# Performance work log

Hardware: AMD Instinct MI355X
Metric: run time of the kernel (lower is better)

## Reference

```python
import jax, jax.numpy as jnp
import numpy as np

B, T, DIM, H = 4, 2048, 1024, 16
HD = DIM // H  # 64
ROPE_BASE = 10000.0


def _rope_cos_sin(seq_len, head_dim, dtype):
    # lucidrains rotary-embedding-torch convention: interleaved pairs.
    inv_freq = 1.0 / (ROPE_BASE ** (jnp.arange(0, head_dim, 2, dtype=jnp.float32) / head_dim))
    freqs = jnp.arange(seq_len, dtype=jnp.float32)[:, None] * inv_freq[None, :]  # [T, hd/2]
    freqs = jnp.repeat(freqs, 2, axis=-1)  # [T, hd], each freq duplicated for the pair
    return jnp.cos(freqs).astype(dtype), jnp.sin(freqs).astype(dtype)


def _rotate_half(x):
    # interleaved pairs: (x1, x2) -> (-x2, x1)
    x = x.reshape(*x.shape[:-1], -1, 2)
    x1, x2 = x[..., 0], x[..., 1]
    return jnp.stack([-x2, x1], axis=-1).reshape(*x.shape[:-2], -1)


def _apply_rope(x, cos, sin):
    # x: [B, H, T, hd]; cos/sin: [T, hd]
    return x * cos[None, None, :, :] + _rotate_half(x) * sin[None, None, :, :]


def setup_inputs() -> dict:
    key = jax.random.key(0)
    kx, kqkv, kw, kb = jax.random.split(key, 4)
    s_qkv = 1.0 / np.sqrt(DIM)
    return {
        "x": jax.random.normal(kx, (B, T, DIM), dtype=jnp.float32),
        "w_qkv": jax.random.normal(kqkv, (3 * DIM, DIM), dtype=jnp.float32) * s_qkv,
        "w_proj": jax.random.normal(kw, (DIM, DIM), dtype=jnp.float32) * s_qkv,
        "b_proj": jax.random.normal(kb, (DIM,), dtype=jnp.float32) * 0.01,
    }


def reference(x, w_qkv, w_proj, b_proj):
    b, t, c = x.shape
    qkv = jnp.einsum('btc,dc->btd', x, w_qkv)  # [B, T, 3*C]
    qkv = qkv.reshape(b, t, 3, H, HD).transpose(2, 0, 3, 1, 4)  # [3, B, H, T, hd]
    q, k, v = qkv[0], qkv[1], qkv[2]

    cos, sin = _rope_cos_sin(t, HD, x.dtype)
    q = _apply_rope(q, cos, sin)
    k = _apply_rope(k, cos, sin)

    scale = 1.0 / np.sqrt(HD)
    scores = jnp.einsum('bhqd,bhkd->bhqk', q, k) * scale  # [B, H, T, T]
    attn = jax.nn.softmax(scores, axis=-1)
    out = jnp.einsum('bhqk,bhkd->bhqd', attn, v)  # [B, H, T, hd]

    out = out.transpose(0, 2, 1, 3).reshape(b, t, c)  # [B, T, C]
    return jnp.einsum('btc,dc->btd', out, w_proj) + b_proj
```

## Files before the change

kernel.cpp:

```cpp
#include <hip/hip_runtime.h>
#include <hip/hip_bf16.h>
#include <math.h>

#define Bz   4
#define Tz   2048
#define DIMz 1024
#define Hz   16
#define HDz  64
#define BHz  (Bz*Hz)
#define Mz   (Bz*Tz)
#define LOG2E 1.44269504088896340736f
#define QSCALE (0.125f * LOG2E)

typedef __attribute__((ext_vector_type(8)))  __bf16 bf16x8;
typedef __attribute__((ext_vector_type(4)))  __bf16 bf16x4;
typedef __attribute__((ext_vector_type(2)))  __bf16 bf16x2;
typedef __attribute__((ext_vector_type(4)))  float  f32x4;
typedef __attribute__((ext_vector_type(16))) float  f32x16;

__device__ __forceinline__ f32x4 mfma_16x16x32(bf16x8 a, bf16x8 b, f32x4 c) {
  return __builtin_amdgcn_mfma_f32_16x16x32_bf16(a, b, c, 0, 0, 0);
}
__device__ __forceinline__ f32x16 mfma_32x32x16(bf16x8 a, bf16x8 b, f32x16 c) {
  return __builtin_amdgcn_mfma_f32_32x32x16_bf16(a, b, c, 0, 0, 0);
}

__device__ __forceinline__ ushort f2bf(float f) {
  unsigned u = __float_as_uint(f);
  u += 0x7fffu + ((u >> 16) & 1u);
  return (ushort)(u >> 16);
}

__device__ __forceinline__ void gl_lds16(const ushort* g, ushort* l) {
  __builtin_amdgcn_global_load_lds(
      (const __attribute__((address_space(1))) unsigned int*)g,
      (__attribute__((address_space(3))) unsigned int*)l, 16, 0, 0);
}

#define N4_X   (Mz * DIMz / 4)
#define N4_WQ  (3 * DIMz * DIMz / 4)
#define N4_WP  (DIMz * DIMz / 4)
__global__ void k_cvt3(const float4* __restrict__ x,  ushort4* __restrict__ ox,
                       const float4* __restrict__ wq, ushort4* __restrict__ owq,
                       const float4* __restrict__ wp, ushort4* __restrict__ owp) {
  int i = blockIdx.x * blockDim.x + threadIdx.x;
  const float4* in; ushort4* out;
  if (i < N4_X)                { in = x + i;                 out = ox + i; }
  else if (i < N4_X + N4_WQ)   { in = wq + (i - N4_X);       out = owq + (i - N4_X); }
  else if (i < N4_X + N4_WQ + N4_WP) { in = wp + (i - N4_X - N4_WQ); out = owp + (i - N4_X - N4_WQ); }
  else return;
  float4 v = *in;
  ushort4 o;
  o.x = f2bf(v.x); o.y = f2bf(v.y); o.z = f2bf(v.z); o.w = f2bf(v.w);
  *out = o;
}

__global__ void k_rope_tab(float* __restrict__ tab) {
  int idx = blockIdx.x * blockDim.x + threadIdx.x;
  if (idx >= Tz * 32) return;
  int t = idx >> 5, i = idx & 31;
  double ang = (double)t * exp(((double)(-2 * i) / (double)HDz) * log(10000.0));
  tab[2 * idx]     = (float)cos(ang);
  tab[2 * idx + 1] = (float)sin(ang);
}


__global__ __launch_bounds__(256) void k_gemm_qkv(const ushort* __restrict__ A,
                                                  const ushort* __restrict__ Bw,
                                                  const float* __restrict__ tab,
                                                  ushort* __restrict__ qb,
                                                  ushort* __restrict__ kb,
                                                  ushort* __restrict__ vbt) {
  __shared__ ushort As[128 * 64];
  __shared__ ushort Bs[128 * 64];
  const int tid = threadIdx.x;
  const int bm = (blockIdx.x & 63) << 7;
  const int bn = (blockIdx.x >> 6) << 7;
  const int wid = tid >> 6, lane = tid & 63;
  const int wr = (wid & 1) << 6, wc = (wid >> 1) << 6;
  const int lr = lane & 15, lg = lane >> 4;

  const int r8 = lane >> 3;
  const int cswz = (((lane & 7) ^ r8) << 3);
  const ushort* pA = A  + (size_t)(bm + wid * 8 + r8) * 1024 + cswz;
  const ushort* pB = Bw + (size_t)(bn + wid * 8 + r8) * 1024 + cswz;
  ushort* lA = &As[wid * 512];
  ushort* lB = &Bs[wid * 512];

  const int cs0 = ((lg ^ (lr & 7)) << 3);
  const int cs1 = cs0 ^ 32;

  const f32x4 fz = {0.f, 0.f, 0.f, 0.f};
  f32x4 acc[4][4];
  #pragma unroll
  for (int i = 0; i < 4; i++)
    #pragma unroll
    for (int j = 0; j < 4; j++) acc[i][j] = fz;

  for (int k0 = 0; k0 < 1024; k0 += 64) {
    __syncthreads();
    #pragma unroll
    for (int rep = 0; rep < 4; rep++) {
      gl_lds16(pA + (size_t)rep * 32768 + k0, lA + rep * 2048);
      gl_lds16(pB + (size_t)rep * 32768 + k0, lB + rep * 2048);
    }
    __syncthreads();
    #pragma unroll
    for (int kc = 0; kc < 2; kc++) {
      const int cs = kc ? cs1 : cs0;
      bf16x8 af[4], bfr[4];
      #pragma unroll
      for (int i = 0; i < 4; i++)
        af[i] = *reinterpret_cast<const bf16x8*>(&As[(wr + i * 16 + lr) * 64 + cs]);
      #pragma unroll
      for (int j = 0; j < 4; j++)
        bfr[j] = *reinterpret_cast<const bf16x8*>(&Bs[(wc + j * 16 + lr) * 64 + cs]);
      #pragma unroll
      for (int i = 0; i < 4; i++)
        #pragma unroll
        for (int j = 0; j < 4; j++)
          acc[i][j] = mfma_16x16x32(af[i], bfr[j], acc[i][j]);
    }
  }

  #pragma unroll
  for (int j = 0; j < 4; j++) {
    int col = bn + wc + j * 16 + lr;
    int which = col >> 10;
    int r = col & 1023;
    int h = r >> 6, hd = r & 63;
    #pragma unroll
    for (int i = 0; i < 4; i++) {
      int row0 = bm + wr + i * 16 + lg * 4;
      int b = row0 >> 11, t0 = row0 & 2047;
      if (which == 2) {
        int t0p = (t0 & ~12) | ((t0 & 4) << 1) | ((t0 & 8) >> 1);
        uint lo = (uint)f2bf(acc[i][j][0]) | ((uint)f2bf(acc[i][j][1]) << 16);
        uint hi = (uint)f2bf(acc[i][j][2]) | ((uint)f2bf(acc[i][j][3]) << 16);
        *reinterpret_cast<uint2*>(&vbt[((size_t)(b * Hz + h) * HDz + hd) * Tz + t0p]) =
            make_uint2(lo, hi);
      } else {
        ushort* dst = (which == 0) ? qb : kb;
        const float sc = (which == 0) ? QSCALE : 1.0f;
        const float sgn = (hd & 1) ? 1.0f : -1.0f;
        const float* tb = &tab[((size_t)t0 * 32 + (hd >> 1)) * 2];
        #pragma unroll
        for (int q = 0; q < 4; q++) {
          float own = acc[i][j][q];
          float other = __shfl_xor(own, 1);
          float c = tb[q * 64], s = tb[q * 64 + 1];
          dst[(((size_t)(b * Hz + h) * Tz + t0 + q) << 6) + hd] =
              f2bf((own * c + sgn * other * s) * sc);
        }
      }
    }
  }
}

__global__ __launch_bounds__(256, 4) void k_attn(const ushort* __restrict__ qb,
                                                 const ushort* __restrict__ kbp,
                                                 const ushort* __restrict__ vbt,
                                                 ushort* __restrict__ ao) {
  __shared__ ushort Ks0[64 * 64], Ks1[64 * 64], Ks2[64 * 64];
  __shared__ ushort Vs0[64 * 64], Vs1[64 * 64];

  const int bid = ((blockIdx.x & 7) << 7) + (blockIdx.x >> 3);
  const int qt = bid & 15;
  const int bh = bid >> 4;
  const int tid = threadIdx.x, wid = tid >> 6, lane = tid & 63;
  const int l31 = lane & 31, hi = lane >> 5;

  const ushort* Kg = kbp + (size_t)bh * Tz * HDz;
  const ushort* Vg = vbt + (size_t)bh * HDz * Tz;

  const ushort* Qrow = qb + ((size_t)bh * Tz + qt * 128 + wid * 32 + l31) * HDz + hi * 8;
  bf16x8 qf[4];
  #pragma unroll
  for (int m = 0; m < 4; m++)
    qf[m] = *reinterpret_cast<const bf16x8*>(Qrow + m * 16);

  bf16x8 onev;
  #pragma unroll
  for (int j = 0; j < 8; j++) onev[j] = (__bf16)1.0f;

  const int r8 = lane >> 3;
  const int c0 = (((lane & 7) ^ r8 ^ ((2 * wid) & 3)) << 3);
  const int c1 = (((lane & 7) ^ r8 ^ ((2 * wid + 1) & 3)) << 3);
  const ushort* kp0 = Kg + (size_t)(wid * 16 + r8) * 64 + c0;
  const ushort* kp1 = Kg + (size_t)(wid * 16 + 8 + r8) * 64 + c1;
  const ushort* vp0 = Vg + (size_t)(wid * 16 + r8) * Tz + c0;
  const ushort* vp1 = Vg + (size_t)(wid * 16 + 8 + r8) * Tz + c1;

  f32x16 oacc0, oacc1, lacc;
  #pragma unroll
  for (int i = 0; i < 16; i++) { oacc0[i] = 0.f; oacc1[i] = 0.f; lacc[i] = 0.f; }

  const int swr = (lane & 7) ^ ((lane >> 3) & 3);
  int csk[4];
  #pragma unroll
  for (int m = 0; m < 4; m++) csk[m] = ((2 * m + hi) ^ swr) << 3;

  union FP { uint u[4]; bf16x8 v; };

  ushort *kb_cur = Ks0, *kb_nxt = Ks1, *kb_pre = Ks2;
  ushort *vb_cur = Vs0, *vb_nxt = Vs1;

  gl_lds16(kp0, kb_cur + wid * 1024); gl_lds16(kp1, kb_cur + wid * 1024 + 512);
  gl_lds16(kp0 + 4096, kb_nxt + wid * 1024); gl_lds16(kp1 + 4096, kb_nxt + wid * 1024 + 512);
  gl_lds16(vp0, vb_cur + wid * 1024); gl_lds16(vp1, vb_cur + wid * 1024 + 512);
  asm volatile("s_waitcnt vmcnt(4)" ::: "memory");
  __builtin_amdgcn_s_barrier();

  const int NT = Tz / 64;
  for (int kt = 0; kt < NT; kt++) {
    if (kt + 2 < NT) {
      gl_lds16(kp0 + (size_t)(kt + 2) * 4096, kb_pre + wid * 1024);
      gl_lds16(kp1 + (size_t)(kt + 2) * 4096, kb_pre + wid * 1024 + 512);
    }

    f32x16 sA, sB;
    #pragma unroll
    for (int i = 0; i < 16; i++) { sA[i] = 0.f; sB[i] = 0.f; }
    __builtin_amdgcn_s_setprio(1);
    #pragma unroll
    for (int m = 0; m < 4; m++) {
      bf16x8 kfA = *reinterpret_cast<const bf16x8*>(&kb_cur[l31 * 64 + csk[m]]);
      bf16x8 kfB = *reinterpret_cast<const bf16x8*>(&kb_cur[(32 + l31) * 64 + csk[m]]);
      sA = mfma_32x32x16(kfA, qf[m], sA);
      sB = mfma_32x32x16(kfB, qf[m], sB);
    }
    __builtin_amdgcn_s_setprio(0);

    FP fA0, fA1, fB0, fB1;
    #pragma unroll
    for (int i = 0; i < 4; i++) {
      bf16x2 a0, a1, b0, b1;
      a0[0] = (__bf16)__builtin_exp2f(sA[2 * i]);
      a0[1] = (__bf16)__builtin_exp2f(sA[2 * i + 1]);
      a1[0] = (__bf16)__builtin_exp2f(sA[8 + 2 * i]);
      a1[1] = (__bf16)__builtin_exp2f(sA[9 + 2 * i]);
      b0[0] = (__bf16)__builtin_exp2f(sB[2 * i]);
      b0[1] = (__bf16)__builtin_exp2f(sB[2 * i + 1]);
      b1[0] = (__bf16)__builtin_exp2f(sB[8 + 2 * i]);
      b1[1] = (__bf16)__builtin_exp2f(sB[9 + 2 * i]);
      fA0.u[i] = *reinterpret_cast<uint*>(&a0);
      fA1.u[i] = *reinterpret_cast<uint*>(&a1);
      fB0.u[i] = *reinterpret_cast<uint*>(&b0);
      fB1.u[i] = *reinterpret_cast<uint*>(&b1);
    }

    asm volatile("s_waitcnt vmcnt(2)" ::: "memory");
    __builtin_amdgcn_s_barrier();

    if (kt + 1 < NT) {
      gl_lds16(vp0 + (kt + 1) * 64, vb_nxt + wid * 1024);
      gl_lds16(vp1 + (kt + 1) * 64, vb_nxt + wid * 1024 + 512);
    }

    __builtin_amdgcn_s_setprio(1);
    lacc = mfma_32x32x16(fA0.v, onev, lacc);
    lacc = mfma_32x32x16(fA1.v, onev, lacc);
    lacc = mfma_32x32x16(fB0.v, onev, lacc);
    lacc = mfma_32x32x16(fB1.v, onev, lacc);
    #pragma unroll
    for (int blk = 0; blk < 2; blk++) {
      const ushort* vrow = &vb_cur[(blk * 32 + l31) * 64];
      bf16x8 vf0 = *reinterpret_cast<const bf16x8*>(vrow + csk[0]);
      bf16x8 vf1 = *reinterpret_cast<const bf16x8*>(vrow + csk[1]);
      bf16x8 vf2 = *reinterpret_cast<const bf16x8*>(vrow + csk[2]);
      bf16x8 vf3 = *reinterpret_cast<const bf16x8*>(vrow + csk[3]);
      f32x16 o = blk ? oacc1 : oacc0;
      o = mfma_32x32x16(fA0.v, vf0, o);
      o = mfma_32x32x16(fA1.v, vf1, o);
      o = mfma_32x32x16(fB0.v, vf2, o);
      o = mfma_32x32x16(fB1.v, vf3, o);
      if (blk) oacc1 = o; else oacc0 = o;
    }
    __builtin_amdgcn_s_setprio(0);

    ushort* t0 = kb_cur; kb_cur = kb_nxt; kb_nxt = kb_pre; kb_pre = t0;
    ushort* t1 = vb_cur; vb_cur = vb_nxt; vb_nxt = t1;
  }

  const int b = bh >> 4, h = bh & 15;
  #pragma unroll
  for (int r = 0; r < 16; r++) {
    int qrow = (r & 3) + 8 * (r >> 2) + 4 * hi;
    int t = qt * 128 + wid * 32 + qrow;
    float inv = 1.0f / lacc[r];
    size_t base = ((size_t)(b * Tz + t) * Hz + h) * HDz;
    ao[base + l31]      = f2bf(oacc0[r] * inv);
    ao[base + 32 + l31] = f2bf(oacc1[r] * inv);
  }
}

__global__ __launch_bounds__(256) void k_gemm_proj(const ushort* __restrict__ A,
                                                   const ushort* __restrict__ Bw,
                                                   const float* __restrict__ bias,
                                                   float* __restrict__ out) {
  __shared__ ushort As[128 * 64];
  __shared__ ushort Bs[128 * 64];
  const int tid = threadIdx.x;
  const int bm = (blockIdx.x & 63) << 7;
  const int bn = (blockIdx.x >> 6) << 7;
  const int wid = tid >> 6, lane = tid & 63;
  const int wr = (wid & 1) << 6, wc = (wid >> 1) << 6;
  const int lr = lane & 15, lg = lane >> 4;

  const int r8 = lane >> 3;
  const int cswz = (((lane & 7) ^ r8) << 3);
  const ushort* pA = A  + (size_t)(bm + wid * 8 + r8) * 1024 + cswz;
  const ushort* pB = Bw + (size_t)(bn + wid * 8 + r8) * 1024 + cswz;
  ushort* lA = &As[wid * 512];
  ushort* lB = &Bs[wid * 512];

  const int cs0 = ((lg ^ (lr & 7)) << 3);
  const int cs1 = cs0 ^ 32;

  const f32x4 fz = {0.f, 0.f, 0.f, 0.f};
  f32x4 acc[4][4];
  #pragma unroll
  for (int i = 0; i < 4; i++)
    #pragma unroll
    for (int j = 0; j < 4; j++) acc[i][j] = fz;

  for (int k0 = 0; k0 < 1024; k0 += 64) {
    __syncthreads();
    #pragma unroll
    for (int rep = 0; rep < 4; rep++) {
      gl_lds16(pA + (size_t)rep * 32768 + k0, lA + rep * 2048);
      gl_lds16(pB + (size_t)rep * 32768 + k0, lB + rep * 2048);
    }
    __syncthreads();
    #pragma unroll
    for (int kc = 0; kc < 2; kc++) {
      const int cs = kc ? cs1 : cs0;
      bf16x8 af[4], bfr[4];
      #pragma unroll
      for (int i = 0; i < 4; i++)
        af[i] = *reinterpret_cast<const bf16x8*>(&As[(wr + i * 16 + lr) * 64 + cs]);
      #pragma unroll
      for (int j = 0; j < 4; j++)
        bfr[j] = *reinterpret_cast<const bf16x8*>(&Bs[(wc + j * 16 + lr) * 64 + cs]);
      #pragma unroll
      for (int i = 0; i < 4; i++)
        #pragma unroll
        for (int j = 0; j < 4; j++)
          acc[i][j] = mfma_16x16x32(af[i], bfr[j], acc[i][j]);
    }
  }

  #pragma unroll
  for (int j = 0; j < 4; j++) {
    int col = bn + wc + j * 16 + lr;
    float bv = bias[col];
    #pragma unroll
    for (int i = 0; i < 4; i++) {
      #pragma unroll
      for (int q = 0; q < 4; q++) {
        int row = bm + wr + i * 16 + lg * 4 + q;
        out[(size_t)row * 1024 + col] = acc[i][j][q] + bv;
      }
    }
  }
}

extern "C" void kernel_launch(void* const* d_in, const int* in_sizes, int n_in,
                              void* d_out, int out_size, void* d_ws, size_t ws_size,
                              hipStream_t stream) {
  const float* x      = (const float*)d_in[0];
  const float* w_qkv  = (const float*)d_in[1];
  const float* w_proj = (const float*)d_in[2];
  const float* b_proj = (const float*)d_in[3];
  float* out = (float*)d_out;

  char* ws = (char*)d_ws;
  ushort* xh     = (ushort*)ws; ws += (size_t)Mz * DIMz * 2;
  ushort* wqkvh  = (ushort*)ws; ws += (size_t)3 * DIMz * DIMz * 2;
  ushort* wprojh = (ushort*)ws; ws += (size_t)DIMz * DIMz * 2;
  ushort* qbuf   = (ushort*)ws; ws += (size_t)BHz * Tz * HDz * 2;
  ushort* kbuf   = (ushort*)ws; ws += (size_t)BHz * Tz * HDz * 2;
  ushort* vbuft  = (ushort*)ws; ws += (size_t)BHz * HDz * Tz * 2;
  ushort* aout   = (ushort*)ws; ws += (size_t)Mz * DIMz * 2;
  float*  tab    = (float*)ws;  ws += (size_t)Tz * 32 * 2 * 4;

  k_cvt3<<<(N4_X + N4_WQ + N4_WP + 255) / 256, 256, 0, stream>>>(
      (const float4*)x, (ushort4*)xh,
      (const float4*)w_qkv, (ushort4*)wqkvh,
      (const float4*)w_proj, (ushort4*)wprojh);
  k_rope_tab<<<256, 256, 0, stream>>>(tab);
  k_gemm_qkv<<<64 * 24, 256, 0, stream>>>(xh, wqkvh, tab, qbuf, kbuf, vbuft);
  k_attn<<<BHz * (Tz / 128), 256, 0, stream>>>(qbuf, kbuf, vbuft, aout);
  k_gemm_proj<<<64 * 8, 256, 0, stream>>>(aout, wprojh, b_proj, out);
}
```

Baseline: 218.0 us.

## Process 64 query rows per wave in attention and compute row sums on VALU

Each wave now handles two 32-row query tiles against the same K/V fragments read from LDS, so each block covers 256 queries and the grid is halved. This doubles the reuse of K/V shared-memory reads per MFMA. The softmax denominator is now accumulated with VALU adds and a cross-half shuffle rather than extra MFMAs against a ones vector, which removes those MFMAs. The cost is more accumulator registers per wave, a launch-bounds occupancy target lowered from 4 to 2, and fewer blocks to spread across the GPU.

Measured after the change: 204.7 us. 6.1% less time.

```diff
diff --git a/kernel.cpp b/kernel.cpp
--- a/kernel.cpp
+++ b/kernel.cpp
@@ -157,31 +157,29 @@
   }
 }
 
-__global__ __launch_bounds__(256, 4) void k_attn(const ushort* __restrict__ qb,
+__global__ __launch_bounds__(256, 2) void k_attn(const ushort* __restrict__ qb,
                                                  const ushort* __restrict__ kbp,
                                                  const ushort* __restrict__ vbt,
                                                  ushort* __restrict__ ao) {
   __shared__ ushort Ks0[64 * 64], Ks1[64 * 64], Ks2[64 * 64];
   __shared__ ushort Vs0[64 * 64], Vs1[64 * 64];
 
-  const int bid = ((blockIdx.x & 7) << 7) + (blockIdx.x >> 3);
-  const int qt = bid & 15;
-  const int bh = bid >> 4;
+  const int bid = ((blockIdx.x & 7) << 6) + (blockIdx.x >> 3);
+  const int qt = bid & 7;
+  const int bh = bid >> 3;
   const int tid = threadIdx.x, wid = tid >> 6, lane = tid & 63;
   const int l31 = lane & 31, hi = lane >> 5;
 
   const ushort* Kg = kbp + (size_t)bh * Tz * HDz;
   const ushort* Vg = vbt + (size_t)bh * HDz * Tz;
 
-  const ushort* Qrow = qb + ((size_t)bh * Tz + qt * 128 + wid * 32 + l31) * HDz + hi * 8;
-  bf16x8 qf[4];
-  #pragma unroll
-  for (int m = 0; m < 4; m++)
-    qf[m] = *reinterpret_cast<const bf16x8*>(Qrow + m * 16);
-
-  bf16x8 onev;
-  #pragma unroll
-  for (int j = 0; j < 8; j++) onev[j] = (__bf16)1.0f;
+  const ushort* Qrow = qb + ((size_t)bh * Tz + qt * 256 + wid * 64 + l31) * HDz + hi * 8;
+  bf16x8 qf0[4], qf1[4];
+  #pragma unroll
+  for (int m = 0; m < 4; m++) {
+    qf0[m] = *reinterpret_cast<const bf16x8*>(Qrow + m * 16);
+    qf1[m] = *reinterpret_cast<const bf16x8*>(Qrow + 32 * HDz + m * 16);
+  }
 
   const int r8 = lane >> 3;
   const int c0 = (((lane & 7) ^ r8 ^ ((2 * wid) & 3)) << 3);
@@ -191,9 +189,10 @@
   const ushort* vp0 = Vg + (size_t)(wid * 16 + r8) * Tz + c0;
   const ushort* vp1 = Vg + (size_t)(wid * 16 + 8 + r8) * Tz + c1;
 
-  f32x16 oacc0, oacc1, lacc;
-  #pragma unroll
-  for (int i = 0; i < 16; i++) { oacc0[i] = 0.f; oacc1[i] = 0.f; lacc[i] = 0.f; }
+  f32x16 oacc00, oacc01, oacc10, oacc11;
+  #pragma unroll
+  for (int i = 0; i < 16; i++) { oacc00[i] = 0.f; oacc01[i] = 0.f; oacc10[i] = 0.f; oacc11[i] = 0.f; }
+  float lrun0 = 0.f, lrun1 = 0.f;
 
   const int swr = (lane & 7) ^ ((lane >> 3) & 3);
   int csk[4];
@@ -218,36 +217,61 @@
       gl_lds16(kp1 + (size_t)(kt + 2) * 4096, kb_pre + wid * 1024 + 512);
     }
 
-    f32x16 sA, sB;
-    #pragma unroll
-    for (int i = 0; i < 16; i++) { sA[i] = 0.f; sB[i] = 0.f; }
+    f32x16 s00, s01, s10, s11;
+    #pragma unroll
+    for (int i = 0; i < 16; i++) { s00[i] = 0.f; s01[i] = 0.f; s10[i] = 0.f; s11[i] = 0.f; }
     __builtin_amdgcn_s_setprio(1);
     #pragma unroll
     for (int m = 0; m < 4; m++) {
       bf16x8 kfA = *reinterpret_cast<const bf16x8*>(&kb_cur[l31 * 64 + csk[m]]);
       bf16x8 kfB = *reinterpret_cast<const bf16x8*>(&kb_cur[(32 + l31) * 64 + csk[m]]);
-      sA = mfma_32x32x16(kfA, qf[m], sA);
-      sB = mfma_32x32x16(kfB, qf[m], sB);
+      s00 = mfma_32x32x16(kfA, qf0[m], s00);
+      s01 = mfma_32x32x16(kfB, qf0[m], s01);
+      s10 = mfma_32x32x16(kfA, qf1[m], s10);
+      s11 = mfma_32x32x16(kfB, qf1[m], s11);
     }
     __builtin_amdgcn_s_setprio(0);
 
-    FP fA0, fA1, fB0, fB1;
+    FP f00, f01, f02, f03, f10, f11, f12, f13;
+    float rs0 = 0.f, rs1 = 0.f;
     #pragma unroll
     for (int i = 0; i < 4; i++) {
-      bf16x2 a0, a1, b0, b1;
-      a0[0] = (__bf16)__builtin_exp2f(sA[2 * i]);
-      a0[1] = (__bf16)__builtin_exp2f(sA[2 * i + 1]);
-      a1[0] = (__bf16)__builtin_exp2f(sA[8 + 2 * i]);
-      a1[1] = (__bf16)__builtin_exp2f(sA[9 + 2 * i]);
-      b0[0] = (__bf16)__builtin_exp2f(sB[2 * i]);
-      b0[1] = (__bf16)__builtin_exp2f(sB[2 * i + 1]);
-      b1[0] = (__bf16)__builtin_exp2f(sB[8 + 2 * i]);
-      b1[1] = (__bf16)__builtin_exp2f(sB[9 + 2 * i]);
-      fA0.u[i] = *reinterpret_cast<uint*>(&a0);
-      fA1.u[i] = *reinterpret_cast<uint*>(&a1);
-      fB0.u[i] = *reinterpret_cast<uint*>(&b0);
-      fB1.u[i] = *reinterpret_cast<uint*>(&b1);
-    }
+      float a0 = __builtin_exp2f(s00[2 * i]),     a1 = __builtin_exp2f(s00[2 * i + 1]);
+      float a2 = __builtin_exp2f(s00[8 + 2 * i]), a3 = __builtin_exp2f(s00[9 + 2 * i]);
+      float b0 = __builtin_exp2f(s01[2 * i]),     b1 = __builtin_exp2f(s01[2 * i + 1]);
+      float b2 = __builtin_exp2f(s01[8 + 2 * i]), b3 = __builtin_exp2f(s01[9 + 2 * i]);
+      rs0 += (a0 + a1) + (a2 + a3) + (b0 + b1) + (b2 + b3);
+      bf16x2 t0, t1, t2, t3;
+      t0[0] = (__bf16)a0; t0[1] = (__bf16)a1;
+      t1[0] = (__bf16)a2; t1[1] = (__bf16)a3;
+      t2[0] = (__bf16)b0; t2[1] = (__bf16)b1;
+      t3[0] = (__bf16)b2; t3[1] = (__bf16)b3;
+      f00.u[i] = *reinterpret_cast<uint*>(&t0);
+      f01.u[i] = *reinterpret_cast<uint*>(&t1);
+      f02.u[i] = *reinterpret_cast<uint*>(&t2);
+      f03.u[i] = *reinterpret_cast<uint*>(&t3);
+    }
+    #pragma unroll
+    for (int i = 0; i < 4; i++) {
+      float a0 = __builtin_exp2f(s10[2 * i]),     a1 = __builtin_exp2f(s10[2 * i + 1]);
+      float a2 = __builtin_exp2f(s10[8 + 2 * i]), a3 = __builtin_exp2f(s10[9 + 2 * i]);
+      float b0 = __builtin_exp2f(s11[2 * i]),     b1 = __builtin_exp2f(s11[2 * i + 1]);
+      float b2 = __builtin_exp2f(s11[8 + 2 * i]), b3 = __builtin_exp2f(s11[9 + 2 * i]);
+      rs1 += (a0 + a1) + (a2 + a3) + (b0 + b1) + (b2 + b3);
+      bf16x2 t0, t1, t2, t3;
+      t0[0] = (__bf16)a0; t0[1] = (__bf16)a1;
+      t1[0] = (__bf16)a2; t1[1] = (__bf16)a3;
+      t2[0] = (__bf16)b0; t2[1] = (__bf16)b1;
+      t3[0] = (__bf16)b2; t3[1] = (__bf16)b3;
+      f10.u[i] = *reinterpret_cast<uint*>(&t0);
+      f11.u[i] = *reinterpret_cast<uint*>(&t1);
+      f12.u[i] = *reinterpret_cast<uint*>(&t2);
+      f13.u[i] = *reinterpret_cast<uint*>(&t3);
+    }
+    rs0 += __shfl_xor(rs0, 32);
+    rs1 += __shfl_xor(rs1, 32);
+    lrun0 += rs0;
+    lrun1 += rs1;
 
     asm volatile("s_waitcnt vmcnt(2)" ::: "memory");
     __builtin_amdgcn_s_barrier();
@@ -258,23 +282,35 @@
     }
 
     __builtin_amdgcn_s_setprio(1);
-    lacc = mfma_32x32x16(fA0.v, onev, lacc);
-    lacc = mfma_32x32x16(fA1.v, onev, lacc);
-    lacc = mfma_32x32x16(fB0.v, onev, lacc);
-    lacc = mfma_32x32x16(fB1.v, onev, lacc);
-    #pragma unroll
-    for (int blk = 0; blk < 2; blk++) {
-      const ushort* vrow = &vb_cur[(blk * 32 + l31) * 64];
-      bf16x8 vf0 = *reinterpret_cast<const bf16x8*>(vrow + csk[0]);
-      bf16x8 vf1 = *reinterpret_cast<const bf16x8*>(vrow + csk[1]);
-      bf16x8 vf2 = *reinterpret_cast<const bf16x8*>(vrow + csk[2]);
-      bf16x8 vf3 = *reinterpret_cast<const bf16x8*>(vrow + csk[3]);
-      f32x16 o = blk ? oacc1 : oacc0;
-      o = mfma_32x32x16(fA0.v, vf0, o);
-      o = mfma_32x32x16(fA1.v, vf1, o);
-      o = mfma_32x32x16(fB0.v, vf2, o);
-      o = mfma_32x32x16(fB1.v, vf3, o);
-      if (blk) oacc1 = o; else oacc0 = o;
+    {
+      const ushort* vr = &vb_cur[l31 * 64];
+      bf16x8 vf0 = *reinterpret_cast<const bf16x8*>(vr + csk[0]);
+      bf16x8 vf1 = *reinterpret_cast<const bf16x8*>(vr + csk[1]);
+      bf16x8 vf2 = *reinterpret_cast<const bf16x8*>(vr + csk[2]);
+      bf16x8 vf3 = *reinterpret_cast<const bf16x8*>(vr + csk[3]);
+      oacc00 = mfma_32x32x16(f00.v, vf0, oacc00);
+      oacc00 = mfma_32x32x16(f01.v, vf1, oacc00);
+      oacc00 = mfma_32x32x16(f02.v, vf2, oacc00);
+      oacc00 = mfma_32x32x16(f03.v, vf3, oacc00);
+      oacc10 = mfma_32x32x16(f10.v, vf0, oacc10);
+      oacc10 = mfma_32x32x16(f11.v, vf1, oacc10);
+      oacc10 = mfma_32x32x16(f12.v, vf2, oacc10);
+      oacc10 = mfma_32x32x16(f13.v, vf3, oacc10);
+    }
+    {
+      const ushort* vr = &vb_cur[(32 + l31) * 64];
+      bf16x8 vf0 = *reinterpret_cast<const bf16x8*>(vr + csk[0]);
+      bf16x8 vf1 = *reinterpret_cast<const bf16x8*>(vr + csk[1]);
+      bf16x8 vf2 = *reinterpret_cast<const bf16x8*>(vr + csk[2]);
+      bf16x8 vf3 = *reinterpret_cast<const bf16x8*>(vr + csk[3]);
+      oacc01 = mfma_32x32x16(f00.v, vf0, oacc01);
+      oacc01 = mfma_32x32x16(f01.v, vf1, oacc01);
+      oacc01 = mfma_32x32x16(f02.v, vf2, oacc01);
+      oacc01 = mfma_32x32x16(f03.v, vf3, oacc01);
+      oacc11 = mfma_32x32x16(f10.v, vf0, oacc11);
+      oacc11 = mfma_32x32x16(f11.v, vf1, oacc11);
+      oacc11 = mfma_32x32x16(f12.v, vf2, oacc11);
+      oacc11 = mfma_32x32x16(f13.v, vf3, oacc11);
     }
     __builtin_amdgcn_s_setprio(0);
 
@@ -282,15 +318,19 @@
     ushort* t1 = vb_cur; vb_cur = vb_nxt; vb_nxt = t1;
   }
 
-  const int b = bh >> 4, h = bh & 15;
+  const int b = bh >> 4, hh = bh & 15;
   #pragma unroll
   for (int r = 0; r < 16; r++) {
     int qrow = (r & 3) + 8 * (r >> 2) + 4 * hi;
-    int t = qt * 128 + wid * 32 + qrow;
-    float inv = 1.0f / lacc[r];
-    size_t base = ((size_t)(b * Tz + t) * Hz + h) * HDz;
-    ao[base + l31]      = f2bf(oacc0[r] * inv);
-    ao[base + 32 + l31] = f2bf(oacc1[r] * inv);
+    float i0 = 1.0f / __shfl(lrun0, qrow);
+    float i1 = 1.0f / __shfl(lrun1, qrow);
+    int t0 = qt * 256 + wid * 64 + qrow;
+    size_t base0 = ((size_t)(b * Tz + t0) * Hz + hh) * HDz;
+    size_t base1 = ((size_t)(b * Tz + t0 + 32) * Hz + hh) * HDz;
+    ao[base0 + l31]      = f2bf(oacc00[r] * i0);
+    ao[base0 + 32 + l31] = f2bf(oacc01[r] * i0);
+    ao[base1 + l31]      = f2bf(oacc10[r] * i1);
+    ao[base1 + 32 + l31] = f2bf(oacc11[r] * i1);
   }
 }
 
@@ -390,6 +430,6 @@
       (const float4*)w_proj, (ushort4*)wprojh);
   k_rope_tab<<<256, 256, 0, stream>>>(tab);
   k_gemm_qkv<<<64 * 24, 256, 0, stream>>>(xh, wqkvh, tab, qbuf, kbuf, vbuft);
-  k_attn<<<BHz * (Tz / 128), 256, 0, stream>>>(qbuf, kbuf, vbuft, aout);
+  k_attn<<<BHz * (Tz / 256), 256, 0, stream>>>(qbuf, kbuf, vbuft, aout);
   k_gemm_proj<<<64 * 8, 256, 0, stream>>>(aout, wprojh, b_proj, out);
 }
```
